# Optimization experiments

Measured on AMD Instinct MI355X. Metric: run time of the kernel, lower is better.

The kernel has to match this reference:

```python
import jax, jax.numpy as jnp
import numpy as np

B, S, D, H = 2, 2048, 1024, 16
DEPTH = D // H


def setup_inputs() -> dict:
    key = jax.random.key(0)
    ks = jax.random.split(key, 8)
    w_scale = 0.02
    # causal mask: 1.0 where attention is NOT allowed (added as mask * -1e9)
    causal = jnp.triu(jnp.ones((S, S), dtype=jnp.float32), k=1)[None, None]  # [1,1,S,S]
    return {
        "q": jax.random.normal(ks[0], (B, S, D), dtype=jnp.float32),
        "k": jax.random.normal(ks[1], (B, S, D), dtype=jnp.float32),
        "v": jax.random.normal(ks[2], (B, S, D), dtype=jnp.float32),
        "mask": causal,
        "Wq": jax.random.normal(ks[3], (D, D), dtype=jnp.float32) * w_scale,
        "bq": jnp.zeros((D,), dtype=jnp.float32),
        "Wk": jax.random.normal(ks[4], (D, D), dtype=jnp.float32) * w_scale,
        "bk": jnp.zeros((D,), dtype=jnp.float32),
        "Wv": jax.random.normal(ks[5], (D, D), dtype=jnp.float32) * w_scale,
        "bv": jnp.zeros((D,), dtype=jnp.float32),
        "Wo": jax.random.normal(ks[6], (D, D), dtype=jnp.float32) * w_scale,
        "bo": jnp.zeros((D,), dtype=jnp.float32),
    }


def _split_heads(x):
    # [B,S,D] -> [B,H,S,depth]
    return x.reshape(B, S, H, DEPTH).transpose(0, 2, 1, 3)


def reference(q, k, v, mask, Wq, bq, Wk, bk, Wv, bv, Wo, bo):
    qh = _split_heads(q @ Wq + bq)
    kh = _split_heads(k @ Wk + bk)
    vh = _split_heads(v @ Wv + bv)
    scale = 1.0 / jnp.sqrt(jnp.asarray(DEPTH, dtype=qh.dtype))
    logits = jnp.einsum('bhqd,bhkd->bhqk', qh, kh) * scale  # [B,H,S,S]
    logits = logits + mask * (-1e9)
    attn = jax.nn.softmax(logits, axis=-1)
    out = jnp.einsum('bhqk,bhkd->bhqd', attn, vh)  # [B,H,S,depth]
    out = out.transpose(0, 2, 1, 3).reshape(B, S, D)
    return out @ Wo + bo
```

## Files before the change

### kernel.cpp

```cpp
#include <hip/hip_runtime.h>


typedef unsigned short u16;
typedef unsigned int u32;

using bf16x8 = __attribute__((ext_vector_type(8))) short;
using f32x4  = __attribute__((ext_vector_type(4))) float;

#define SEQ 2048
#define DMODEL 1024
#define NHEAD 16
#define DEPTH 64
#define BATCH 2
#define M_ROWS (BATCH * SEQ)

__device__ __forceinline__ u16 f2bf(float f) {
    union { float f; u32 u; } v; v.f = f;
    u32 u = v.u;
    return (u16)((u + 0x7FFFu + ((u >> 16) & 1u)) >> 16);
}
__device__ __forceinline__ u16 f2bf_trunc(float f) {
    union { float f; u32 u; } v; v.f = f;
    return (u16)(v.u >> 16);
}

__device__ __forceinline__ f32x4 mfma16(bf16x8 a, bf16x8 b, f32x4 c) {
    return __builtin_amdgcn_mfma_f32_16x16x32_bf16(a, b, c, 0, 0, 0);
}

__device__ __forceinline__ void glds16(const u16* src, u16* dst) {
    __builtin_amdgcn_global_load_lds((const __attribute__((address_space(1))) void*)src,
                                     (__attribute__((address_space(3))) void*)dst,
                                     16, 0, 0);
}

__device__ __forceinline__ bf16x8 fragld(const u16* base, int lr, int gc) {
    return *(const bf16x8*)(base + lr * 64 + (((gc ^ lr) & 7) << 3));
}

__global__ void cvt3_kernel(const float* __restrict__ q, const float* __restrict__ k,
                            const float* __restrict__ v,
                            u16* __restrict__ qo, u16* __restrict__ ko, u16* __restrict__ vo) {
    const float* in; u16* out;
    if (blockIdx.z == 0)      { in = q; out = qo; }
    else if (blockIdx.z == 1) { in = k; out = ko; }
    else                      { in = v; out = vo; }
    int idx = blockIdx.x * blockDim.x + threadIdx.x;
    float4 val = ((const float4*)in)[idx];
    ushort4 o;
    o.x = f2bf(val.x); o.y = f2bf(val.y); o.z = f2bf(val.z); o.w = f2bf(val.w);
    ((ushort4*)out)[idx] = o;
}

__global__ void wtrans_kernel(const float* __restrict__ Wq, const float* __restrict__ Wk,
                              const float* __restrict__ Wv, const float* __restrict__ Wo,
                              u16* __restrict__ Wqt, u16* __restrict__ Wkt,
                              u16* __restrict__ Wvt, u16* __restrict__ Wot) {
    __shared__ float tile[32][33];
    const float* W; u16* Wt;
    switch (blockIdx.z) {
        case 0: W = Wq; Wt = Wqt; break;
        case 1: W = Wk; Wt = Wkt; break;
        case 2: W = Wv; Wt = Wvt; break;
        default: W = Wo; Wt = Wot; break;
    }
    int k0 = blockIdx.x * 32, n0 = blockIdx.y * 32;
    int tx = threadIdx.x, ty = threadIdx.y;
#pragma unroll
    for (int i = 0; i < 4; ++i)
        tile[ty + 8 * i][tx] = W[(size_t)(k0 + ty + 8 * i) * DMODEL + n0 + tx];
    __syncthreads();
#pragma unroll
    for (int i = 0; i < 4; ++i)
        Wt[(size_t)(n0 + ty + 8 * i) * DMODEL + k0 + tx] = f2bf(tile[tx][ty + 8 * i]);
}

template<int TM>
__device__ __forceinline__ void gemm_core(const u16* __restrict__ A, const u16* __restrict__ Bt,
                                          const float* __restrict__ bias,
                                          u16* __restrict__ outb, float* __restrict__ outf,
                                          int mode, float oscale, int bm0, int bn0) {
    constexpr int K = DMODEL;
    constexpr int MI = TM / 32;
    __shared__ u16 As[TM * 64];
    __shared__ u16 Bs[128 * 64];
    int t = threadIdx.x;
    int w = t >> 6, lane = t & 63, l15 = lane & 15, quad = lane >> 4;
    int wm = (w >> 1) * (TM / 2), wn = (w & 1) * 64;
    int r8 = lane >> 3, g8 = lane & 7;
    int gswz = ((g8 ^ r8) << 3);
    f32x4 acc[MI][4] = {};

    for (int it = 0; it < K / 64; ++it) {
        int k0 = it * 64;
        __syncthreads();
#pragma unroll
        for (int c = 0; c < MI; ++c) {
            int ch = w * MI + c;
            glds16(A + (size_t)(bm0 + ch * 8 + r8) * K + k0 + gswz, As + ch * 512);
        }
#pragma unroll
        for (int c = 0; c < 4; ++c) {
            int ch = w * 4 + c;
            glds16(Bt + (size_t)(bn0 + ch * 8 + r8) * K + k0 + gswz, Bs + ch * 512);
        }
        __syncthreads();
#pragma unroll
        for (int kk = 0; kk < 2; ++kk) {
            bf16x8 af[MI], bfr[4];
#pragma unroll
            for (int i = 0; i < MI; ++i) af[i]  = fragld(As, wm + i * 16 + l15, kk * 4 + quad);
#pragma unroll
            for (int j = 0; j < 4;  ++j) bfr[j] = fragld(Bs, wn + j * 16 + l15, kk * 4 + quad);
#pragma unroll
            for (int i = 0; i < MI; ++i)
#pragma unroll
                for (int j = 0; j < 4; ++j)
                    acc[i][j] = mfma16(af[i], bfr[j], acc[i][j]);
        }
    }
#pragma unroll
    for (int i = 0; i < MI; ++i) {
        int row_g0 = bm0 + wm + i * 16 + quad * 4;
#pragma unroll
        for (int j = 0; j < 4; ++j) {
            int col_g = bn0 + wn + j * 16 + l15;
            float bsv = bias[col_g];
#pragma unroll
            for (int r = 0; r < 4; ++r) {
                float v = (acc[i][j][r] + bsv) * oscale;
                int rg = row_g0 + r;
                if (mode == 2) {
                    outf[(size_t)rg * DMODEL + col_g] = v;
                } else {
                    int b = rg >> 11, s = rg & (SEQ - 1);
                    int h = col_g >> 6, d = col_g & 63;
                    size_t idx;
                    if (mode == 0) idx = ((size_t)(b * NHEAD + h) * SEQ + s) * DEPTH + d;
                    else           idx = ((size_t)(b * NHEAD + h) * DEPTH + d) * SEQ + s;
                    outb[idx] = f2bf(v);
                }
            }
        }
    }
}

#define SCALE_Q 0.1803368801111204f

__global__ __launch_bounds__(256) void gemm_qkv(
        const u16* __restrict__ qb, const u16* __restrict__ kb, const u16* __restrict__ vb,
        const u16* __restrict__ Wqt, const u16* __restrict__ Wkt, const u16* __restrict__ Wvt,
        const float* __restrict__ bq, const float* __restrict__ bk, const float* __restrict__ bv,
        u16* __restrict__ Qp, u16* __restrict__ Kp, u16* __restrict__ Vpt) {
    int id = blockIdx.x;
    int c = id & 7, m = id >> 3;
    int slab = c * 12 + (m >> 3);
    int x = m & 7;
    int z = slab >> 5, y = slab & 31;
    int bm0 = y * 128, bn0 = x * 128;
    if (z == 0)      gemm_core<128>(qb, Wqt, bq, Qp,  nullptr, 0, SCALE_Q, bm0, bn0);
    else if (z == 1) gemm_core<128>(kb, Wkt, bk, Kp,  nullptr, 0, 1.0f,    bm0, bn0);
    else             gemm_core<128>(vb, Wvt, bv, Vpt, nullptr, 1, 1.0f,    bm0, bn0);
}

__global__ __launch_bounds__(256) void gemm_out(
        const u16* __restrict__ attnb, const u16* __restrict__ Wot,
        const float* __restrict__ bo, float* __restrict__ out) {
    int id = blockIdx.x;
    int c = id & 7, m = id >> 3;
    int slab = c * 8 + (m >> 3);
    int x = m & 7;
    gemm_core<64>(attnb, Wot, bo, nullptr, out, 2, 1.0f, slab * 64, x * 128);
}

#define LP 72
__global__ __launch_bounds__(256) void attn_kernel(
        const u16* __restrict__ Qp, const u16* __restrict__ Kp,
        const u16* __restrict__ Vpt, u16* __restrict__ attn_out, u32* __restrict__ ctrs) {
    __shared__ u16 Klds[2][64 * 64];
    __shared__ u16 Vtlds[2][64 * 64];
    __shared__ u16 Plds[4 * 16 * LP];
    __shared__ u32 item_s;
    int t = threadIdx.x, w = t >> 6, lane = t & 63, l15 = lane & 15, quad = lane >> 4;
    int r8 = lane >> 3, g8 = lane & 7;
    int gswz = ((g8 ^ r8) << 3);
    u16* Pw = Plds + w * 16 * LP;
    int xcd = blockIdx.x & 7;
    u32* my_ctr = ctrs + xcd * 32;

    bf16x8 ones;
#pragma unroll
    for (int i = 0; i < 8; ++i) ones[i] = (short)0x3F80;

    for (;;) {
        if (t == 0) item_s = atomicAdd(my_ctr, 1);
        __syncthreads();
        u32 item = item_s;
        if (item >= 128) break;
        int qt = 31 - (int)(item >> 2);
        int bh = xcd * 4 + (int)(item & 3);
        int q0 = qt * 64;
        int nkt = qt + 1;
        int b = bh >> 4, h = bh & 15;
        const u16* Qbase = Qp  + (size_t)bh * SEQ * DEPTH;
        const u16* Kbase = Kp  + (size_t)bh * SEQ * DEPTH;
        const u16* Vbase = Vpt + (size_t)bh * DEPTH * SEQ;

        int qrow = q0 + w * 16 + l15;
        bf16x8 qf[2];
        qf[0] = *(const bf16x8*)(Qbase + (size_t)qrow * DEPTH + quad * 8);
        qf[1] = *(const bf16x8*)(Qbase + (size_t)qrow * DEPTH + 32 + quad * 8);

        f32x4 of[4] = {};
        f32x4 lacc = {};

#pragma unroll
        for (int c2 = 0; c2 < 2; ++c2) {
            int ch = w * 2 + c2;
            glds16(Kbase + (size_t)(ch * 8 + r8) * DEPTH + gswz, Klds[0] + ch * 512);
            glds16(Vbase + (size_t)(ch * 8 + r8) * SEQ + gswz,   Vtlds[0] + ch * 512);
        }

        for (int kt = 0; kt < nkt; ++kt) {
            int cur = kt & 1;
            __syncthreads();
            if (kt + 1 < nkt) {
                int nx = cur ^ 1, kn = kt + 1;
#pragma unroll
                for (int c2 = 0; c2 < 2; ++c2) {
                    int ch = w * 2 + c2;
                    glds16(Kbase + (size_t)(kn * 64 + ch * 8 + r8) * DEPTH + gswz,
                           Klds[nx] + ch * 512);
                    glds16(Vbase + (size_t)(ch * 8 + r8) * SEQ + kn * 64 + gswz,
                           Vtlds[nx] + ch * 512);
                }
            }
            f32x4 sc[4] = {};
#pragma unroll
            for (int nt = 0; nt < 4; ++nt)
#pragma unroll
                for (int kk = 0; kk < 2; ++kk)
                    sc[nt] = mfma16(qf[kk], fragld(Klds[cur], nt * 16 + l15, kk * 4 + quad), sc[nt]);

            bool diag = (kt == nkt - 1);
#pragma unroll
            for (int nt = 0; nt < 4; ++nt) {
#pragma unroll
                for (int r = 0; r < 4; ++r) {
                    float e = exp2f(sc[nt][r]);
                    if (diag) {
                        int col = nt * 16 + l15, row_ = w * 16 + quad * 4 + r;
                        e = (col > row_) ? 0.f : e;
                    }
                    Pw[(quad * 4 + r) * LP + nt * 16 + l15] = f2bf_trunc(e);
                }
            }
            bf16x8 pf[2];
            pf[0] = *(const bf16x8*)(Pw + l15 * LP + quad * 8);
            pf[1] = *(const bf16x8*)(Pw + l15 * LP + 32 + quad * 8);
#pragma unroll
            for (int kk = 0; kk < 2; ++kk) {
                lacc = mfma16(pf[kk], ones, lacc);
#pragma unroll
                for (int nt = 0; nt < 4; ++nt)
                    of[nt] = mfma16(pf[kk], fragld(Vtlds[cur], nt * 16 + l15, kk * 4 + quad), of[nt]);
            }
        }
#pragma unroll
        for (int r = 0; r < 4; ++r) {
            float inv = 1.0f / lacc[r];
            int s_ = q0 + w * 16 + quad * 4 + r;
#pragma unroll
            for (int nt = 0; nt < 4; ++nt) {
                int dcol = h * DEPTH + nt * 16 + l15;
                attn_out[((size_t)(b * SEQ + s_)) * DMODEL + dcol] = f2bf(of[nt][r] * inv);
            }
        }
    }
}

extern "C" void kernel_launch(void* const* d_in, const int* in_sizes, int n_in,
                              void* d_out, int out_size, void* d_ws, size_t ws_size,
                              hipStream_t stream) {
    const float* q  = (const float*)d_in[0];
    const float* k  = (const float*)d_in[1];
    const float* v  = (const float*)d_in[2];
    const float* Wq = (const float*)d_in[4];
    const float* bq = (const float*)d_in[5];
    const float* Wk = (const float*)d_in[6];
    const float* bk = (const float*)d_in[7];
    const float* Wv = (const float*)d_in[8];
    const float* bv = (const float*)d_in[9];
    const float* Wo = (const float*)d_in[10];
    const float* bo = (const float*)d_in[11];
    float* out = (float*)d_out;

    char* ws = (char*)d_ws;
    const size_t SZ_ACT = (size_t)M_ROWS * DMODEL * 2;
    const size_t SZ_W   = (size_t)DMODEL * DMODEL * 2;
    u16* qb   = (u16*)(ws);
    u16* kb   = (u16*)(ws + SZ_ACT);
    u16* vb   = (u16*)(ws + 2 * SZ_ACT);
    u16* Wqt  = (u16*)(ws + 3 * SZ_ACT);
    u16* Wkt  = (u16*)(ws + 3 * SZ_ACT + SZ_W);
    u16* Wvt  = (u16*)(ws + 3 * SZ_ACT + 2 * SZ_W);
    u16* Wot  = (u16*)(ws + 3 * SZ_ACT + 3 * SZ_W);
    u16* Qp   = (u16*)(ws + 3 * SZ_ACT + 4 * SZ_W);
    u16* Kp   = (u16*)(ws + 4 * SZ_ACT + 4 * SZ_W);
    u16* Vpt  = (u16*)(ws + 5 * SZ_ACT + 4 * SZ_W);
    u16* attnb= (u16*)(ws + 6 * SZ_ACT + 4 * SZ_W);
    u32* ctrs = (u32*)(ws + 7 * SZ_ACT + 4 * SZ_W);

    hipMemsetAsync(ctrs, 0, 1024, stream);
    cvt3_kernel<<<dim3(4096, 1, 3), 256, 0, stream>>>(q, k, v, qb, kb, vb);
    wtrans_kernel<<<dim3(32, 32, 4), dim3(32, 8), 0, stream>>>(Wq, Wk, Wv, Wo, Wqt, Wkt, Wvt, Wot);
    gemm_qkv<<<dim3(768), 256, 0, stream>>>(
        qb, kb, vb, Wqt, Wkt, Wvt, bq, bk, bv, Qp, Kp, Vpt);
    attn_kernel<<<dim3(768), 256, 0, stream>>>(Qp, Kp, Vpt, attnb, ctrs);
    gemm_out<<<dim3(512), 256, 0, stream>>>(attnb, Wot, bo, out);
}
```

Baseline: 237.2 us.

## Use 32x32 MFMA with 128-row query tiles in attention kernel

The attention kernel moves from 16x16x32 to 32x32x16 bf16 MFMA and has each wave own 32 query rows, so a block covers 128 query rows. Each K/V tile loaded into LDS is therefore reused by twice as many queries, and the number of work items drops from 128 to 64 per XCD counter. In exchange there are fewer items to balance across CUs, more accumulator registers per wave, and a larger P staging buffer. Causal masking now applies to the last two key tiles.

```diff
diff --git a/kernel.cpp b/kernel.cpp
--- a/kernel.cpp
+++ b/kernel.cpp
@@ -6,6 +6,7 @@
 
 using bf16x8 = __attribute__((ext_vector_type(8))) short;
 using f32x4  = __attribute__((ext_vector_type(4))) float;
+using f32x16 = __attribute__((ext_vector_type(16))) float;
 
 #define SEQ 2048
 #define DMODEL 1024
@@ -26,6 +27,9 @@
 
 __device__ __forceinline__ f32x4 mfma16(bf16x8 a, bf16x8 b, f32x4 c) {
     return __builtin_amdgcn_mfma_f32_16x16x32_bf16(a, b, c, 0, 0, 0);
+}
+__device__ __forceinline__ f32x16 mfma32(bf16x8 a, bf16x8 b, f32x16 c) {
+    return __builtin_amdgcn_mfma_f32_32x32x16_bf16(a, b, c, 0, 0, 0);
 }
 
 __device__ __forceinline__ void glds16(const u16* src, u16* dst) {
@@ -173,18 +177,19 @@
     gemm_core<64>(attnb, Wot, bo, nullptr, out, 2, 1.0f, slab * 64, x * 128);
 }
 
-#define LP 72
+#define LPW 68
 __global__ __launch_bounds__(256) void attn_kernel(
         const u16* __restrict__ Qp, const u16* __restrict__ Kp,
         const u16* __restrict__ Vpt, u16* __restrict__ attn_out, u32* __restrict__ ctrs) {
     __shared__ u16 Klds[2][64 * 64];
     __shared__ u16 Vtlds[2][64 * 64];
-    __shared__ u16 Plds[4 * 16 * LP];
+    __shared__ u16 Plds[4 * 32 * LPW];
     __shared__ u32 item_s;
-    int t = threadIdx.x, w = t >> 6, lane = t & 63, l15 = lane & 15, quad = lane >> 4;
+    int t = threadIdx.x, w = t >> 6, lane = t & 63;
+    int l31 = lane & 31, half = lane >> 5;
     int r8 = lane >> 3, g8 = lane & 7;
     int gswz = ((g8 ^ r8) << 3);
-    u16* Pw = Plds + w * 16 * LP;
+    u16* Pw = Plds + w * 32 * LPW;
     int xcd = blockIdx.x & 7;
     u32* my_ctr = ctrs + xcd * 32;
 
@@ -196,23 +201,25 @@
         if (t == 0) item_s = atomicAdd(my_ctr, 1);
         __syncthreads();
         u32 item = item_s;
-        if (item >= 128) break;
-        int qt = 31 - (int)(item >> 2);
+        if (item >= 64) break;
+        int qt = 15 - (int)(item >> 2);
         int bh = xcd * 4 + (int)(item & 3);
-        int q0 = qt * 64;
-        int nkt = qt + 1;
+        int q0 = qt * 128;
+        int nkt = 2 * qt + 2;
         int b = bh >> 4, h = bh & 15;
         const u16* Qbase = Qp  + (size_t)bh * SEQ * DEPTH;
         const u16* Kbase = Kp  + (size_t)bh * SEQ * DEPTH;
         const u16* Vbase = Vpt + (size_t)bh * DEPTH * SEQ;
 
-        int qrow = q0 + w * 16 + l15;
-        bf16x8 qf[2];
-        qf[0] = *(const bf16x8*)(Qbase + (size_t)qrow * DEPTH + quad * 8);
-        qf[1] = *(const bf16x8*)(Qbase + (size_t)qrow * DEPTH + 32 + quad * 8);
-
-        f32x4 of[4] = {};
-        f32x4 lacc = {};
+        bf16x8 qf[4];
+        {
+            const u16* qp = Qbase + (size_t)(q0 + w * 32 + l31) * DEPTH + half * 8;
+#pragma unroll
+            for (int kk = 0; kk < 4; ++kk) qf[kk] = *(const bf16x8*)(qp + kk * 16);
+        }
+
+        f32x16 of[2] = {};
+        f32x16 lacc = {};
 
 #pragma unroll
         for (int c2 = 0; c2 < 2; ++c2) {
@@ -235,45 +242,52 @@
                            Vtlds[nx] + ch * 512);
                 }
             }
-            f32x4 sc[4] = {};
-#pragma unroll
-            for (int nt = 0; nt < 4; ++nt)
-#pragma unroll
-                for (int kk = 0; kk < 2; ++kk)
-                    sc[nt] = mfma16(qf[kk], fragld(Klds[cur], nt * 16 + l15, kk * 4 + quad), sc[nt]);
-
-            bool diag = (kt == nkt - 1);
-#pragma unroll
-            for (int nt = 0; nt < 4; ++nt) {
-#pragma unroll
-                for (int r = 0; r < 4; ++r) {
-                    float e = exp2f(sc[nt][r]);
-                    if (diag) {
-                        int col = nt * 16 + l15, row_ = w * 16 + quad * 4 + r;
-                        e = (col > row_) ? 0.f : e;
+            f32x16 sc[2] = {};
+#pragma unroll
+            for (int nt = 0; nt < 2; ++nt)
+#pragma unroll
+                for (int kk = 0; kk < 4; ++kk)
+                    sc[nt] = mfma32(qf[kk],
+                                    fragld(Klds[cur], nt * 32 + l31, kk * 2 + half), sc[nt]);
+
+            bool tail = (kt >= nkt - 2);
+#pragma unroll
+            for (int nt = 0; nt < 2; ++nt) {
+#pragma unroll
+                for (int reg = 0; reg < 16; ++reg) {
+                    int rowC = (reg & 3) + 8 * (reg >> 2) + 4 * half;
+                    float e = exp2f(sc[nt][reg]);
+                    if (tail) {
+                        int colg = kt * 64 + nt * 32 + l31;
+                        int rowg = q0 + w * 32 + rowC;
+                        e = (colg > rowg) ? 0.f : e;
                     }
-                    Pw[(quad * 4 + r) * LP + nt * 16 + l15] = f2bf_trunc(e);
+                    Pw[rowC * LPW + nt * 32 + l31] = f2bf_trunc(e);
                 }
             }
-            bf16x8 pf[2];
-            pf[0] = *(const bf16x8*)(Pw + l15 * LP + quad * 8);
-            pf[1] = *(const bf16x8*)(Pw + l15 * LP + 32 + quad * 8);
-#pragma unroll
-            for (int kk = 0; kk < 2; ++kk) {
-                lacc = mfma16(pf[kk], ones, lacc);
-#pragma unroll
-                for (int nt = 0; nt < 4; ++nt)
-                    of[nt] = mfma16(pf[kk], fragld(Vtlds[cur], nt * 16 + l15, kk * 4 + quad), of[nt]);
-            }
-        }
-#pragma unroll
-        for (int r = 0; r < 4; ++r) {
-            float inv = 1.0f / lacc[r];
-            int s_ = q0 + w * 16 + quad * 4 + r;
-#pragma unroll
-            for (int nt = 0; nt < 4; ++nt) {
-                int dcol = h * DEPTH + nt * 16 + l15;
-                attn_out[((size_t)(b * SEQ + s_)) * DMODEL + dcol] = f2bf(of[nt][r] * inv);
+            bf16x8 pf[4];
+#pragma unroll
+            for (int kk = 0; kk < 4; ++kk)
+                pf[kk] = *(const bf16x8*)(Pw + l31 * LPW + kk * 16 + half * 8);
+#pragma unroll
+            for (int kk = 0; kk < 4; ++kk)
+                lacc = mfma32(pf[kk], ones, lacc);
+#pragma unroll
+            for (int nt = 0; nt < 2; ++nt)
+#pragma unroll
+                for (int kk = 0; kk < 4; ++kk)
+                    of[nt] = mfma32(pf[kk],
+                                    fragld(Vtlds[cur], nt * 32 + l31, kk * 2 + half), of[nt]);
+        }
+#pragma unroll
+        for (int reg = 0; reg < 16; ++reg) {
+            int rowC = (reg & 3) + 8 * (reg >> 2) + 4 * half;
+            float inv = 1.0f / lacc[reg];
+            int s_ = q0 + w * 32 + rowC;
+#pragma unroll
+            for (int nt = 0; nt < 2; ++nt) {
+                int dcol = h * DEPTH + nt * 32 + l31;
+                attn_out[((size_t)(b * SEQ + s_)) * DMODEL + dcol] = f2bf(of[nt][reg] * inv);
             }
         }
     }
```

New measurement: 267.8 us. +12.9%, slower.
